# Optimization experiments

Hardware: AMD Instinct MI355X
Metric: run time of the kernel (lower is better)

## Reference

```python
import jax, jax.numpy as jnp
import numpy as np

N_NODES = 100000
N_EDGES = 3200000
D_FEAT = 256
N_CHANNELS = 256


def setup_inputs() -> dict:
    key = jax.random.key(0)
    ks = jax.random.split(key, 7)
    features = jax.random.normal(ks[0], (N_NODES, D_FEAT), dtype=jnp.float32)
    edge_rows = jax.random.randint(ks[1], (N_EDGES,), 0, N_NODES, dtype=jnp.int32)
    edge_cols = jax.random.randint(ks[2], (N_EDGES,), 0, N_NODES, dtype=jnp.int32)
    # normalized adjacency values ~ 1/degree scale
    edge_vals = jax.random.uniform(ks[3], (N_EDGES,), dtype=jnp.float32) / 32.0
    kernel = jax.random.normal(ks[4], (D_FEAT, N_CHANNELS), dtype=jnp.float32) * (1.0 / np.sqrt(D_FEAT))
    bias = jax.random.normal(ks[5], (N_CHANNELS,), dtype=jnp.float32) * 0.01
    skip_weight = jax.random.normal(ks[6], (N_CHANNELS,), dtype=jnp.float32)
    return {
        "features": features,
        "edge_rows": edge_rows,
        "edge_cols": edge_cols,
        "edge_vals": edge_vals,
        "kernel": kernel,
        "bias": bias,
        "skip_weight": skip_weight,
    }


def reference(features, edge_rows, edge_cols, edge_vals, kernel, bias, skip_weight):
    # dense projection: [n, d] @ [d, c] -> [n, c]
    h = features @ kernel
    # SpMM with COO adjacency: out[r] += vals[e] * h[c] for edge e=(r,c)
    gathered = edge_vals[:, None] * h[edge_cols]            # [E, c]
    agg = jax.ops.segment_sum(gathered, edge_rows, num_segments=N_NODES)  # [n, c]
    # skip connection + bias + activation (selu)
    out = h * skip_weight + agg + bias
    return jax.nn.selu(out)
```

## Files before the change

### kernel.cpp

```cpp
#include <hip/hip_runtime.h>
#include <hip/hip_bf16.h>

#define N_NODES 100000
#define N_EDGES 3200000
#define D 256
#define CAP 96

typedef __attribute__((ext_vector_type(8))) short short8;
typedef __attribute__((ext_vector_type(4))) float f32x4;

__device__ __forceinline__ float selu_f(float x) {
    const float SCALE = 1.0507009873554805f;
    const float ALPHA = 1.6732632423543772f;
    return SCALE * (x > 0.f ? x : ALPHA * expm1f(x));
}

__device__ __forceinline__ ushort f2bf(float f) {
    unsigned int u = __float_as_uint(f);
    u += 0x7FFFu + ((u >> 16) & 1u);
    return (ushort)(u >> 16);
}

__device__ __forceinline__ float bflo(unsigned int u) { return __uint_as_float(u << 16); }
__device__ __forceinline__ float bfhi(unsigned int u) { return __uint_as_float(u & 0xFFFF0000u); }

__global__ __launch_bounds__(256) void k_convert(const float* __restrict__ X,
                                                 ushort* __restrict__ Xb) {
    int i = blockIdx.x * 256 + threadIdx.x;
    const int n4 = N_NODES * D / 4;
    if (i < n4) {
        float4 v = ((const float4*)X)[i];
        ushort4 o;
        o.x = f2bf(v.x); o.y = f2bf(v.y); o.z = f2bf(v.z); o.w = f2bf(v.w);
        ((ushort4*)Xb)[i] = o;
    }
}

__global__ __launch_bounds__(256) void k_wt(const float* __restrict__ W,
                                            ushort* __restrict__ Wt) {
    int idx = blockIdx.x * 256 + threadIdx.x;
    int n = idx >> 8, k = idx & 255;
    Wt[n * 256 + k] = f2bf(W[k * 256 + n]);
}

__global__ __launch_bounds__(256) void k_mfma(const ushort* __restrict__ Xb,
                                              const ushort* __restrict__ Wt,
                                              ushort* __restrict__ Hb) {
    __shared__ ushort As[128][72];
    __shared__ ushort Bs[128][72];
    const int t    = threadIdx.x;
    const int lane = t & 63;
    const int wid  = t >> 6;
    const int wr   = wid >> 1;
    const int wc   = wid & 1;
    const int m0   = blockIdx.x * 128;
    const int n0   = blockIdx.y * 128;
    const int lrow = lane & 15;
    const int lk   = (lane >> 4) * 8;

    f32x4 acc[4][4] = {};

    for (int kt = 0; kt < 256; kt += 64) {
#pragma unroll
        for (int p = 0; p < 4; ++p) {
            int idx = p * 256 + t;
            int row = idx >> 3;
            int kc  = (idx & 7) * 8;
            int grow = m0 + row;
            short8 va = {0, 0, 0, 0, 0, 0, 0, 0};
            if (grow < N_NODES)
                va = *(const short8*)(Xb + (size_t)grow * 256 + kt + kc);
            *(short8*)&As[row][kc] = va;
            short8 vb = *(const short8*)(Wt + (size_t)(n0 + row) * 256 + kt + kc);
            *(short8*)&Bs[row][kc] = vb;
        }
        __syncthreads();
#pragma unroll
        for (int kk = 0; kk < 64; kk += 32) {
            short8 a[4], b[4];
#pragma unroll
            for (int ai = 0; ai < 4; ++ai)
                a[ai] = *(const short8*)&As[wr * 64 + ai * 16 + lrow][kk + lk];
#pragma unroll
            for (int bj = 0; bj < 4; ++bj)
                b[bj] = *(const short8*)&Bs[wc * 64 + bj * 16 + lrow][kk + lk];
#pragma unroll
            for (int ai = 0; ai < 4; ++ai)
#pragma unroll
                for (int bj = 0; bj < 4; ++bj)
                    acc[ai][bj] = __builtin_amdgcn_mfma_f32_16x16x32_bf16(
                        a[ai], b[bj], acc[ai][bj], 0, 0, 0);
        }
        __syncthreads();
    }

    const int crow = (lane >> 4) * 4;
    const int ccol = lane & 15;
#pragma unroll
    for (int ai = 0; ai < 4; ++ai)
#pragma unroll
        for (int r = 0; r < 4; ++r) {
            int grow = m0 + wr * 64 + ai * 16 + crow + r;
            if (grow < N_NODES) {
#pragma unroll
                for (int bj = 0; bj < 4; ++bj) {
                    int gcol = n0 + wc * 64 + bj * 16 + ccol;
                    Hb[(size_t)grow * 256 + gcol] = f2bf(acc[ai][bj][r]);
                }
            }
        }
}

__global__ __launch_bounds__(256) void k_scatter(const int4* __restrict__ rows4,
                                                 const int4* __restrict__ cols4,
                                                 const float4* __restrict__ vals4,
                                                 int* __restrict__ cursor,
                                                 int2* __restrict__ cedge) {
    int q = blockIdx.x * 256 + threadIdx.x;
    if (q < N_EDGES / 4) {
        int4   r = rows4[q];
        int4   c = cols4[q];
        float4 v = vals4[q];
        int p0 = atomicAdd(&cursor[r.x], 1);
        int p1 = atomicAdd(&cursor[r.y], 1);
        int p2 = atomicAdd(&cursor[r.z], 1);
        int p3 = atomicAdd(&cursor[r.w], 1);
        if (p0 < CAP) cedge[(size_t)r.x * CAP + p0] = make_int2(c.x, __float_as_int(v.x));
        if (p1 < CAP) cedge[(size_t)r.y * CAP + p1] = make_int2(c.y, __float_as_int(v.y));
        if (p2 < CAP) cedge[(size_t)r.z * CAP + p2] = make_int2(c.z, __float_as_int(v.z));
        if (p3 < CAP) cedge[(size_t)r.w * CAP + p3] = make_int2(c.w, __float_as_int(v.w));
    }
}

__global__ __launch_bounds__(256) void k_spmm(const int* __restrict__ cursor,
                                              const int2* __restrict__ cedge,
                                              const uint2* __restrict__ H2,
                                              const float* __restrict__ bias,
                                              const float* __restrict__ skw,
                                              float* __restrict__ out) {
    const int r    = blockIdx.x * 4 + (threadIdx.x >> 6);
    const int lane = threadIdx.x & 63;
    float a0 = 0.f, a1 = 0.f, a2 = 0.f, a3 = 0.f;
    int deg = cursor[r];
    if (deg > CAP) deg = CAP;
    const size_t rbase = (size_t)r * CAP;
    for (int base = 0; base < deg; base += 64) {
        int n = deg - base;
        if (n > 64) n = 64;
        int2 e = make_int2(0, 0);
        if (lane < n) e = cedge[rbase + base + lane];
        int i = 0;
        for (; i + 4 <= n; i += 4) {
            int   c0 = __shfl(e.x, i);     float v0 = __int_as_float(__shfl(e.y, i));
            int   c1 = __shfl(e.x, i + 1); float v1 = __int_as_float(__shfl(e.y, i + 1));
            int   c2 = __shfl(e.x, i + 2); float v2 = __int_as_float(__shfl(e.y, i + 2));
            int   c3 = __shfl(e.x, i + 3); float v3 = __int_as_float(__shfl(e.y, i + 3));
            uint2 u0 = H2[(size_t)c0 * 64 + lane];
            uint2 u1 = H2[(size_t)c1 * 64 + lane];
            uint2 u2 = H2[(size_t)c2 * 64 + lane];
            uint2 u3 = H2[(size_t)c3 * 64 + lane];
            a0 = fmaf(v0, bflo(u0.x), a0); a1 = fmaf(v0, bfhi(u0.x), a1);
            a2 = fmaf(v0, bflo(u0.y), a2); a3 = fmaf(v0, bfhi(u0.y), a3);
            a0 = fmaf(v1, bflo(u1.x), a0); a1 = fmaf(v1, bfhi(u1.x), a1);
            a2 = fmaf(v1, bflo(u1.y), a2); a3 = fmaf(v1, bfhi(u1.y), a3);
            a0 = fmaf(v2, bflo(u2.x), a0); a1 = fmaf(v2, bfhi(u2.x), a1);
            a2 = fmaf(v2, bflo(u2.y), a2); a3 = fmaf(v2, bfhi(u2.y), a3);
            a0 = fmaf(v3, bflo(u3.x), a0); a1 = fmaf(v3, bfhi(u3.x), a1);
            a2 = fmaf(v3, bflo(u3.y), a2); a3 = fmaf(v3, bfhi(u3.y), a3);
        }
        for (; i < n; ++i) {
            int   c0 = __shfl(e.x, i);
            float v0 = __int_as_float(__shfl(e.y, i));
            uint2 u0 = H2[(size_t)c0 * 64 + lane];
            a0 = fmaf(v0, bflo(u0.x), a0); a1 = fmaf(v0, bfhi(u0.x), a1);
            a2 = fmaf(v0, bflo(u0.y), a2); a3 = fmaf(v0, bfhi(u0.y), a3);
        }
    }
    uint2  hu = H2[(size_t)r * 64 + lane];
    float4 sw = *(const float4*)&skw[4 * lane];
    float4 bs = *(const float4*)&bias[4 * lane];
    float4 o;
    o.x = selu_f(fmaf(bflo(hu.x), sw.x, a0 + bs.x));
    o.y = selu_f(fmaf(bfhi(hu.x), sw.y, a1 + bs.y));
    o.z = selu_f(fmaf(bflo(hu.y), sw.z, a2 + bs.z));
    o.w = selu_f(fmaf(bfhi(hu.y), sw.w, a3 + bs.w));
    *(float4*)&out[(size_t)r * D + 4 * lane] = o;
}

extern "C" void kernel_launch(void* const* d_in, const int* in_sizes, int n_in,
                              void* d_out, int out_size, void* d_ws, size_t ws_size,
                              hipStream_t stream) {
    const float* X     = (const float*)d_in[0];
    const int*   erows = (const int*)d_in[1];
    const int*   ecols = (const int*)d_in[2];
    const float* evals = (const float*)d_in[3];
    const float* W     = (const float*)d_in[4];
    const float* bias  = (const float*)d_in[5];
    const float* skw   = (const float*)d_in[6];
    float* out = (float*)d_out;

    char* ws = (char*)d_ws;
    size_t off = 0;
    auto alloc = [&](size_t bytes) -> void* {
        void* p = ws + off;
        off += (bytes + 255) & ~(size_t)255;
        return p;
    };
    ushort* Xb     = (ushort*)alloc((size_t)N_NODES * D * 2);
    ushort* Wt     = (ushort*)alloc((size_t)D * D * 2);
    ushort* Hb     = (ushort*)alloc((size_t)N_NODES * D * 2);
    int*    cursor = (int*)alloc((size_t)N_NODES * 4);
    int2*   cedge  = (int2*)alloc((size_t)N_NODES * CAP * 8);

    hipMemsetAsync(cursor, 0, (size_t)N_NODES * 4, stream);

    k_convert<<<(N_NODES * D / 4 + 255) / 256, 256, 0, stream>>>(X, Xb);
    k_wt<<<D * D / 256, 256, 0, stream>>>(W, Wt);
    k_mfma<<<dim3((N_NODES + 127) / 128, 2), 256, 0, stream>>>(Xb, Wt, Hb);

    k_scatter<<<(N_EDGES / 4 + 255) / 256, 256, 0, stream>>>(
        (const int4*)erows, (const int4*)ecols, (const float4*)evals, cursor, cedge);

    k_spmm<<<N_NODES / 4, 256, 0, stream>>>(cursor, cedge,
                                            (const uint2*)Hb, bias, skw, out);
}
```

Before: 678.9 us.

## Partition edge scatter by destination-row group to localize atomics and writes

Result: faster. 610.1 us (-10.1%).

```diff
diff --git a/kernel.cpp b/kernel.cpp
--- a/kernel.cpp
+++ b/kernel.cpp
@@ -5,6 +5,8 @@
 #define N_EDGES 3200000
 #define D 256
 #define CAP 96
+#define NGROUP 8
+#define ROWS_PER_G 12500
 
 typedef __attribute__((ext_vector_type(8))) short short8;
 typedef __attribute__((ext_vector_type(4))) float f32x4;
@@ -116,19 +118,31 @@
                                                  const float4* __restrict__ vals4,
                                                  int* __restrict__ cursor,
                                                  int2* __restrict__ cedge) {
-    int q = blockIdx.x * 256 + threadIdx.x;
-    if (q < N_EDGES / 4) {
-        int4   r = rows4[q];
-        int4   c = cols4[q];
-        float4 v = vals4[q];
-        int p0 = atomicAdd(&cursor[r.x], 1);
-        int p1 = atomicAdd(&cursor[r.y], 1);
-        int p2 = atomicAdd(&cursor[r.z], 1);
-        int p3 = atomicAdd(&cursor[r.w], 1);
-        if (p0 < CAP) cedge[(size_t)r.x * CAP + p0] = make_int2(c.x, __float_as_int(v.x));
-        if (p1 < CAP) cedge[(size_t)r.y * CAP + p1] = make_int2(c.y, __float_as_int(v.y));
-        if (p2 < CAP) cedge[(size_t)r.z * CAP + p2] = make_int2(c.z, __float_as_int(v.z));
-        if (p3 < CAP) cedge[(size_t)r.w * CAP + p3] = make_int2(c.w, __float_as_int(v.w));
+    const int group = blockIdx.x & (NGROUP - 1);
+    const int rlo   = group * ROWS_PER_G;
+    const int qbase = (blockIdx.x >> 3) * 512 + threadIdx.x;
+#pragma unroll
+    for (int it = 0; it < 2; ++it) {
+        int q = qbase + it * 256;
+        if (q < N_EDGES / 4) {
+            int4 r = rows4[q];
+            bool o0 = (unsigned)(r.x - rlo) < (unsigned)ROWS_PER_G;
+            bool o1 = (unsigned)(r.y - rlo) < (unsigned)ROWS_PER_G;
+            bool o2 = (unsigned)(r.z - rlo) < (unsigned)ROWS_PER_G;
+            bool o3 = (unsigned)(r.w - rlo) < (unsigned)ROWS_PER_G;
+            if (o0 | o1 | o2 | o3) {
+                int4   c = cols4[q];
+                float4 v = vals4[q];
+                if (o0) { int p = atomicAdd(&cursor[r.x], 1);
+                          if (p < CAP) cedge[(size_t)r.x * CAP + p] = make_int2(c.x, __float_as_int(v.x)); }
+                if (o1) { int p = atomicAdd(&cursor[r.y], 1);
+                          if (p < CAP) cedge[(size_t)r.y * CAP + p] = make_int2(c.y, __float_as_int(v.y)); }
+                if (o2) { int p = atomicAdd(&cursor[r.z], 1);
+                          if (p < CAP) cedge[(size_t)r.z * CAP + p] = make_int2(c.z, __float_as_int(v.z)); }
+                if (o3) { int p = atomicAdd(&cursor[r.w], 1);
+                          if (p < CAP) cedge[(size_t)r.w * CAP + p] = make_int2(c.w, __float_as_int(v.w)); }
+            }
+        }
     }
 }
 
@@ -218,7 +232,7 @@
     k_wt<<<D * D / 256, 256, 0, stream>>>(W, Wt);
     k_mfma<<<dim3((N_NODES + 127) / 128, 2), 256, 0, stream>>>(Xb, Wt, Hb);
 
-    k_scatter<<<(N_EDGES / 4 + 255) / 256, 256, 0, stream>>>(
+    k_scatter<<<NGROUP * 1563, 256, 0, stream>>>(
         (const int4*)erows, (const int4*)ecols, (const float4*)evals, cursor, cedge);
 
     k_spmm<<<N_NODES / 4, 256, 0, stream>>>(cursor, cedge,
```
